# Performance work log

Hardware: AMD Instinct MI355X
Metric: run time of the kernel (lower is better)

Reference implementation:

```python
import jax, jax.numpy as jnp
import numpy as np

B, N, P, D, NH, DFFN = 4, 1024, 128, 512, 8, 2048
DH = D // NH  # 64


def setup_inputs() -> dict:
    key = jax.random.key(0)
    ks = jax.random.split(key, 64)
    i = [0]
    def rn(shape, s=1.0):
        k = ks[i[0]]; i[0] += 1
        return jax.random.normal(k, shape, jnp.float32) * s
    w = 0.05  # weight init scale
    inp = {
        "H": rn((B, N, D)),
        "V": rn((B, N, 3, D)),
        "D_batch": rn((B, N, N)),
        "rbf_bias": rn((B, 1, N, N)),  # rbf_feat_batch[layer_idx]
        "prompt_feature": rn((B * P, D)),
        # self-attn params
        "Wq": rn((4 * D, D), w), "bq": jnp.zeros((4 * D,), jnp.float32),
        "Wk": rn((4 * D, D), w), "bk": jnp.zeros((4 * D,), jnp.float32),
        "Wv": rn((D, D), w), "bv": jnp.zeros((D,), jnp.float32),
        "Wvv": rn((D, D), w),
        "Wo": rn((D, D), w), "bo": jnp.zeros((D,), jnp.float32),
        "Wvo": rn((D, D), w),
        "ln1_g": jnp.ones((D,), jnp.float32), "ln1_b": jnp.zeros((D,), jnp.float32),
        # cross-attn params (nn.MultiheadAttention packed in_proj + out_proj, then scaler_o)
        "ca_in_w": rn((3 * D, D), w), "ca_in_b": jnp.zeros((3 * D,), jnp.float32),
        "ca_out_w": rn((D, D), w), "ca_out_b": jnp.zeros((D,), jnp.float32),
        "ca_so_w": rn((D, D), w), "ca_so_b": jnp.zeros((D,), jnp.float32),
        "ln2_g": jnp.ones((D,), jnp.float32), "ln2_b": jnp.zeros((D,), jnp.float32),
        # GVP-FFN params
        "ffn_lv": rn((2 * D, D), w),
        "ffn_w1": rn((DFFN, 2 * D), w), "ffn_b1": jnp.zeros((DFFN,), jnp.float32),
        "ffn_w2": rn((2 * D, DFFN), w), "ffn_b2": jnp.zeros((2 * D,), jnp.float32),
        "ln3_g": jnp.ones((D,), jnp.float32), "ln3_b": jnp.zeros((D,), jnp.float32),
        # key-validity mask [B,N]
        "H_mask": jax.random.randint(ks[60], (B, N), 0, 2).astype(jnp.int32),
    }
    return inp


def _ln(x, g, b):
    m = x.mean(-1, keepdims=True)
    v = ((x - m) ** 2).mean(-1, keepdims=True)
    return (x - m) / jnp.sqrt(v + 1e-5) * g + b


def _ept_layer(H, V, D_batch, rbf_bias, prompt_feature,
               Wq, bq, Wk, bk, Wv, bv, Wvv, Wo, bo, Wvo, ln1_g, ln1_b,
               ca_in_w, ca_in_b, ca_out_w, ca_out_b, ca_so_w, ca_so_b, ln2_g, ln2_b,
               ffn_lv, ffn_w1, ffn_b1, ffn_w2, ffn_b2, ln3_g, ln3_b, H_mask):
    factor = 0.5 / np.sqrt(DH)
    # ---- self-attn sublayer (pre-LN on H, residual on H and V) ----
    H0, V0 = H, V
    Hn = _ln(H, ln1_g, ln1_b)
    Hq = (Hn @ Wq.T + bq).reshape(B, N, NH, 4 * DH)
    Hk = (Hn @ Wk.T + bk).reshape(B, N, NH, 4 * DH)
    Hv = (Hn @ Wv.T + bv).reshape(B, N, NH, DH)
    # vector values: [B,N,3,D] -> [B,N,3,NH,DH] -> [B,N,NH,3,DH] -> [B,N,NH,3*DH]
    Vv = (V @ Wvv.T).reshape(B, N, 3, NH, DH).transpose(0, 1, 3, 2, 4).reshape(B, N, NH, 3 * DH)
    V_attn = jnp.concatenate([Hv, Vv], axis=-1)  # [B,N,NH,4*DH]
    bias = rbf_bias + D_batch[:, None]           # [B,1,N,N]
    bias = jnp.where(H_mask[:, None, None, :] == 0, -jnp.inf, bias)
    scores = jnp.einsum('bnhd,bmhd->bhnm', Hq, Hk) * factor + bias
    attn = jax.nn.softmax(scores, axis=-1)
    res = jnp.einsum('bhnm,bmhd->bnhd', attn, V_attn)  # [B,N,NH,4*DH]
    H_res = res[..., :DH].reshape(B, N, D)
    V_res = res[..., DH:].reshape(B, N, NH, 3, DH).transpose(0, 1, 3, 2, 4).reshape(B, N, 3, D)
    H = (H_res @ Wo.T + bo) + H0
    V = (V_res @ Wvo.T) + V0
    # ---- cross-attn sublayer (pre-LN, residual on H only) ----
    H0 = H
    Hn = _ln(H, ln2_g, ln2_b)
    prompt = prompt_feature.reshape(B, P, D)
    Wq_c, Wk_c, Wv_c = ca_in_w[:D], ca_in_w[D:2 * D], ca_in_w[2 * D:]
    bq_c, bk_c, bv_c = ca_in_b[:D], ca_in_b[D:2 * D], ca_in_b[2 * D:]
    q = (Hn @ Wq_c.T + bq_c).reshape(B, N, NH, DH)
    k = (prompt @ Wk_c.T + bk_c).reshape(B, P, NH, DH)
    v = (prompt @ Wv_c.T + bv_c).reshape(B, P, NH, DH)
    ca = jax.nn.softmax(jnp.einsum('bnhd,bphd->bhnp', q, k) / np.sqrt(DH), axis=-1)
    co = jnp.einsum('bhnp,bphd->bnhd', ca, v).reshape(B, N, D)
    co = co @ ca_out_w.T + ca_out_b
    H = (co @ ca_so_w.T + ca_so_b) + H0
    # ---- GVP-FFN sublayer (pre-LN on H, residual on H and V) ----
    H0, V0 = H, V
    Hn = _ln(H, ln3_g, ln3_b)
    Vp = V @ ffn_lv.T                  # [B,N,3,2D]
    V1, V2 = Vp[..., :D], Vp[..., D:]
    scaler = jnp.concatenate([Hn, jnp.linalg.norm(V1, axis=-2)], axis=-1)  # [B,N,2D]
    h1 = jax.nn.silu(scaler @ ffn_w1.T + ffn_b1)
    so = h1 @ ffn_w2.T + ffn_b2        # [B,N,2D]
    H_out, V_upd = so[..., :D], so[..., D:]
    H = H_out + H0
    V = V_upd[..., None, :] * V2 + V0  # vector_act == 'none'
    return H, V


def reference(H, V, D_batch, rbf_bias, prompt_feature,
              Wq, bq, Wk, bk, Wv, bv, Wvv, Wo, bo, Wvo, ln1_g, ln1_b,
              ca_in_w, ca_in_b, ca_out_w, ca_out_b, ca_so_w, ca_so_b, ln2_g, ln2_b,
              ffn_lv, ffn_w1, ffn_b1, ffn_w2, ffn_b2, ln3_g, ln3_b, H_mask):
    return _ept_layer(H, V, D_batch, rbf_bias, prompt_feature,
                      Wq, bq, Wk, bk, Wv, bv, Wvv, Wo, bo, Wvo, ln1_g, ln1_b,
                      ca_in_w, ca_in_b, ca_out_w, ca_out_b, ca_so_w, ca_so_b, ln2_g, ln2_b,
                      ffn_lv, ffn_w1, ffn_b1, ffn_w2, ffn_b2, ln3_g, ln3_b, H_mask)
```

## Files before the change

### kernel.cpp

```cpp
#include <hip/hip_runtime.h>
#include <cstdint>
#include <cstddef>

#define B_    4
#define N_    1024
#define P_    128
#define D_    512
#define NH_   8

typedef unsigned short ushort_t;
typedef short short8 __attribute__((ext_vector_type(8)));
typedef float f32x4 __attribute__((ext_vector_type(4)));
typedef ushort_t ushort4_t __attribute__((ext_vector_type(4)));

__device__ inline ushort_t f2bf(float f) {
  union { float fp; unsigned int u; } v; v.fp = f;
  unsigned int r = v.u + 0x7fffu + ((v.u >> 16) & 1u);
  return (ushort_t)(r >> 16);
}
__device__ inline float bf2f(ushort_t u) {
  union { unsigned int i; float f; } v; v.i = ((unsigned int)u) << 16;
  return v.f;
}

__device__ __forceinline__ void gll16(const ushort_t* g, ushort_t* l) {
  __builtin_amdgcn_global_load_lds(
      (const __attribute__((address_space(1))) void*)g,
      (__attribute__((address_space(3))) void*)l, 16, 0, 0);
}

__device__ inline void cast8(const float* __restrict__ s, ushort_t* __restrict__ d,
                             unsigned i) {
  const float* sp = s + (size_t)i * 8;
  short8 o;
#pragma unroll
  for (int j = 0; j < 8; ++j) o[j] = (short)f2bf(sp[j]);
  *(short8*)(d + (size_t)i * 8) = o;
}

__global__ __launch_bounds__(256) void cast_fused(
    const float* s0, ushort_t* d0,  const float* s1, ushort_t* d1,
    const float* s2, ushort_t* d2,  const float* s3, ushort_t* d3,
    const float* s4, ushort_t* d4,  const float* s5, ushort_t* d5,
    const float* s6, ushort_t* d6,  const float* s7, ushort_t* d7,
    const float* s8, ushort_t* d8,  const float* s9, ushort_t* d9,
    const float* s10, ushort_t* d10, const float* s11, ushort_t* d11,
    const float* s12, ushort_t* d12, const float* s13, ushort_t* d13)
{
  unsigned i = blockIdx.x * 256 + threadIdx.x;
#define SEG(s, d, n8) if (i < (n8)) { cast8(s, d, i); return; } i -= (n8);
  SEG(s0, d0, 131072u)
  SEG(s1, d1, 131072u)
  SEG(s2, d2, 32768u)
  SEG(s3, d3, 32768u)
  SEG(s4, d4, 32768u)
  SEG(s5, d5, 32768u)
  SEG(s6, d6, 98304u)
  SEG(s7, d7, 32768u)
  SEG(s8, d8, 32768u)
  SEG(s9, d9, 65536u)
  SEG(s10, d10, 262144u)
  SEG(s11, d11, 262144u)
  SEG(s12, d12, 32768u)
  SEG(s13, d13, 786432u)
#undef SEG
}

__global__ __launch_bounds__(256) void biasmerge(const float* __restrict__ bq,
                                                 const float* __restrict__ bk,
                                                 float* __restrict__ o)
{
  int i = blockIdx.x * 256 + threadIdx.x;
  o[i] = (i < 2048) ? bq[i] : bk[i - 2048];
}

__global__ __launch_bounds__(256) void biascomb(const float* __restrict__ Db,
                                                const float* __restrict__ rbf,
                                                const int* __restrict__ mask,
                                                ushort_t* __restrict__ out)
{
  size_t i = (size_t)blockIdx.x * 256 + threadIdx.x;
  size_t e = i * 4;
  int b  = (int)(e >> 20);
  int m0 = (int)(e & 1023);
  float4 r = *(const float4*)(rbf + e);
  float4 d = *(const float4*)(Db + e);
  const int* mp = mask + b * 1024 + m0;
  ushort4_t o;
  o.x = f2bf(mp[0] ? r.x + d.x : -1e30f);
  o.y = f2bf(mp[1] ? r.y + d.y : -1e30f);
  o.z = f2bf(mp[2] ? r.z + d.z : -1e30f);
  o.w = f2bf(mp[3] ? r.w + d.w : -1e30f);
  *(ushort4_t*)(out + e) = o;
}

__global__ __launch_bounds__(256) void ln_kernel(
    const float* __restrict__ x, const float* __restrict__ g,
    const float* __restrict__ bb, ushort_t* __restrict__ y, int ostride)
{
  int row = blockIdx.x;
  int t = threadIdx.x;
  const float* xr = x + (size_t)row * D_;
  float a = xr[t], c = xr[t + 256];
  float s = a + c, sq = a * a + c * c;
#pragma unroll
  for (int off = 32; off >= 1; off >>= 1) {
    s  += __shfl_xor(s, off);
    sq += __shfl_xor(sq, off);
  }
  __shared__ float red[8];
  int w = t >> 6, lane = t & 63;
  if (lane == 0) { red[w] = s; red[4 + w] = sq; }
  __syncthreads();
  float st  = red[0] + red[1] + red[2] + red[3];
  float sqt = red[4] + red[5] + red[6] + red[7];
  float mean = st * (1.0f / D_);
  float var  = sqt * (1.0f / D_) - mean * mean;
  float inv  = rsqrtf(var + 1e-5f);
  y[(size_t)row * ostride + t]       = f2bf((a - mean) * inv * g[t] + bb[t]);
  y[(size_t)row * ostride + t + 256] = f2bf((c - mean) * inv * g[t + 256] + bb[t + 256]);
}

__global__ __launch_bounds__(256) void gemm_bf16(
    const ushort_t* __restrict__ A, const ushort_t* __restrict__ W,
    const float* __restrict__ bias, const float* __restrict__ res,
    float* __restrict__ Cf, ushort_t* __restrict__ Cb,
    int M, int N, int K, int flags)
{
  __shared__ __align__(16) ushort_t Al[128 * 32];
  __shared__ __align__(16) ushort_t Wl[128 * 32];
  const int t = threadIdx.x;
  const int wv = t >> 6, lane = t & 63, lr = lane & 15, lk = lane >> 4;
  const int wr = wv >> 1, wc = wv & 1;

  const int gx = gridDim.x;
  const int lid = blockIdx.y * gx + blockIdx.x;
  const int cpx = (gx * gridDim.y) >> 3;
  const int nlid = (lid & 7) * cpx + (lid >> 3);
  const size_t row0 = (size_t)(nlid / gx) * 128;
  const size_t col0 = (size_t)(nlid % gx) * 128;

  const int srow = 32 * wv + (lane >> 2);
  const int scol = (((lane & 3) ^ ((lane >> 3) & 3))) * 8;
  const ushort_t* ApG = A + (row0 + srow) * (size_t)K + scol;
  const ushort_t* WpG = W + (col0 + srow) * (size_t)K + scol;
  ushort_t* AlD = Al + (size_t)(32 * wv) * 32;
  ushort_t* WlD = Wl + (size_t)(32 * wv) * 32;
  const size_t K16 = (size_t)16 * K;

  f32x4 acc[4][4];
#pragma unroll
  for (int i = 0; i < 4; ++i)
#pragma unroll
    for (int j = 0; j < 4; ++j) acc[i][j] = f32x4{0.f, 0.f, 0.f, 0.f};

  const int sx = (lr >> 1) & 3;

  for (int k0 = 0; k0 < K; k0 += 32) {
    __syncthreads();
    gll16(ApG + k0,       AlD);
    gll16(ApG + k0 + K16, AlD + 512);
    gll16(WpG + k0,       WlD);
    gll16(WpG + k0 + K16, WlD + 512);
    __syncthreads();
    short8 af[4], bf[4];
#pragma unroll
    for (int i = 0; i < 4; ++i)
      af[i] = *(const short8*)&Al[(wr * 64 + i * 16 + lr) * 32 + ((lk ^ sx) << 3)];
#pragma unroll
    for (int j = 0; j < 4; ++j)
      bf[j] = *(const short8*)&Wl[(wc * 64 + j * 16 + lr) * 32 + ((lk ^ sx) << 3)];
#pragma unroll
    for (int i = 0; i < 4; ++i)
#pragma unroll
      for (int j = 0; j < 4; ++j)
        acc[i][j] = __builtin_amdgcn_mfma_f32_16x16x32_bf16(af[i], bf[j], acc[i][j], 0, 0, 0);
  }

  const int orow = wr * 64 + lk * 4, ocol = wc * 64 + lr;
#pragma unroll
  for (int i = 0; i < 4; ++i) {
#pragma unroll
    for (int j = 0; j < 4; ++j) {
      size_t colb = col0 + ocol + j * 16;
      float bv = (flags & 1) ? bias[colb] : 0.f;
#pragma unroll
      for (int r = 0; r < 4; ++r) {
        size_t rowg = row0 + orow + i * 16 + r;
        float v = acc[i][j][r] + bv;
        if (flags & 4) v = v / (1.f + __expf(-v));
        if (flags & 2) v += res[rowg * N + colb];
        if (flags & 8)  Cf[rowg * N + colb] = v;
        if (flags & 16) Cb[rowg * N + colb] = f2bf(v);
      }
    }
  }
}

__global__ __launch_bounds__(256) void gemm_bf16_sm(
    const ushort_t* __restrict__ A, const ushort_t* __restrict__ W,
    const float* __restrict__ bias, const float* __restrict__ res,
    float* __restrict__ Cf, ushort_t* __restrict__ Cb,
    int M, int N, int K, int flags)
{
  __shared__ __align__(16) ushort_t Al[64 * 32];
  __shared__ __align__(16) ushort_t Wl[128 * 32];
  const int t = threadIdx.x;
  const int wv = t >> 6, lane = t & 63, lr = lane & 15, lk = lane >> 4;
  const int wr = wv >> 1, wc = wv & 1;

  const int gx = gridDim.x;
  const int lid = blockIdx.y * gx + blockIdx.x;
  const int cpx = (gx * gridDim.y) >> 3;
  const int nlid = (lid & 7) * cpx + (lid >> 3);
  const size_t row0 = (size_t)(nlid / gx) * 64;
  const size_t col0 = (size_t)(nlid % gx) * 128;

  const int scol = (((lane & 3) ^ ((lane >> 3) & 3))) * 8;
  const int srowA = 16 * wv + (lane >> 2);
  const int srowW = 32 * wv + (lane >> 2);
  const ushort_t* ApG = A + (row0 + srowA) * (size_t)K + scol;
  const ushort_t* WpG = W + (col0 + srowW) * (size_t)K + scol;
  ushort_t* AlD = Al + (size_t)(16 * wv) * 32;
  ushort_t* WlD = Wl + (size_t)(32 * wv) * 32;
  const size_t K16 = (size_t)16 * K;

  f32x4 acc[2][4];
#pragma unroll
  for (int i = 0; i < 2; ++i)
#pragma unroll
    for (int j = 0; j < 4; ++j) acc[i][j] = f32x4{0.f, 0.f, 0.f, 0.f};

  const int sx = (lr >> 1) & 3;

  for (int k0 = 0; k0 < K; k0 += 32) {
    __syncthreads();
    gll16(ApG + k0,       AlD);
    gll16(WpG + k0,       WlD);
    gll16(WpG + k0 + K16, WlD + 512);
    __syncthreads();
    short8 af[2], bf[4];
#pragma unroll
    for (int i = 0; i < 2; ++i)
      af[i] = *(const short8*)&Al[(wr * 32 + i * 16 + lr) * 32 + ((lk ^ sx) << 3)];
#pragma unroll
    for (int j = 0; j < 4; ++j)
      bf[j] = *(const short8*)&Wl[(wc * 64 + j * 16 + lr) * 32 + ((lk ^ sx) << 3)];
#pragma unroll
    for (int i = 0; i < 2; ++i)
#pragma unroll
      for (int j = 0; j < 4; ++j)
        acc[i][j] = __builtin_amdgcn_mfma_f32_16x16x32_bf16(af[i], bf[j], acc[i][j], 0, 0, 0);
  }

  const int orow = wr * 32 + lk * 4, ocol = wc * 64 + lr;
#pragma unroll
  for (int i = 0; i < 2; ++i) {
#pragma unroll
    for (int j = 0; j < 4; ++j) {
      size_t colb = col0 + ocol + j * 16;
      float bv = (flags & 1) ? bias[colb] : 0.f;
#pragma unroll
      for (int r = 0; r < 4; ++r) {
        size_t rowg = row0 + orow + i * 16 + r;
        float v = acc[i][j][r] + bv;
        if (flags & 4) v = v / (1.f + __expf(-v));
        if (flags & 2) v += res[rowg * N + colb];
        if (flags & 8)  Cf[rowg * N + colb] = v;
        if (flags & 16) Cb[rowg * N + colb] = f2bf(v);
      }
    }
  }
}

__global__ __launch_bounds__(256) void vt_build(
    const ushort_t* __restrict__ HVb, const ushort_t* __restrict__ VVTb,
    ushort_t* __restrict__ VT)
{
  const int bh = blockIdx.z, b = bh >> 3, h = bh & 7;
  const int n0 = blockIdx.x * 64, dt = blockIdx.y;
  __shared__ __align__(16) ushort_t tile[64][72];
  const int t = threadIdx.x;
  {
    int r = t >> 2, c0 = (t & 3) * 16;
    const ushort_t* src = (dt == 0)
      ? HVb + ((size_t)(b * 1024 + n0 + r)) * 512 + h * 64 + c0
      : VVTb + (((size_t)(b * 1024 + n0 + r)) * 3 + (dt - 1)) * 512 + h * 64 + c0;
    *(short8*)&tile[r][c0]     = *(const short8*)src;
    *(short8*)&tile[r][c0 + 8] = *(const short8*)(src + 8);
  }
  __syncthreads();
  {
    int d = t >> 2, nc = (t & 3) * 16;
    short8 o0, o1;
#pragma unroll
    for (int i = 0; i < 8; ++i) { o0[i] = tile[nc + i][d]; o1[i] = tile[nc + 8 + i][d]; }
    ushort_t* dst = VT + ((size_t)bh * 256 + dt * 64 + d) * 1024 + n0 + nc;
    *(short8*)dst = o0;
    *(short8*)(dst + 8) = o1;
  }
}

__global__ __launch_bounds__(256) void attn_mfma(
    const ushort_t* __restrict__ QKg, const ushort_t* __restrict__ VTg,
    const ushort_t* __restrict__ biasb,
    ushort_t* __restrict__ HRESb, ushort_t* __restrict__ VRESb)
{
  const int bh = blockIdx.y, b = bh >> 3, h = bh & 7;
  const int q0 = blockIdx.x * 64;
  const int t = threadIdx.x, w = t >> 6, lane = t & 63, lr = lane & 15, lk = lane >> 4;

  __shared__ __align__(16) ushort_t Kl[32][264];
  __shared__ __align__(16) ushort_t Vl[256][40];
  __shared__ __align__(16) ushort_t Pl[4][16][40];

  short8 qf[8];
  {
    const ushort_t* qb = QKg + ((size_t)(b * 1024 + q0 + w * 16 + lr)) * 4096 + h * 256;
#pragma unroll
    for (int s = 0; s < 8; ++s) qf[s] = *(const short8*)(qb + s * 32 + lk * 8);
  }
  f32x4 o[16];
#pragma unroll
  for (int i = 0; i < 16; ++i) o[i] = f32x4{0.f, 0.f, 0.f, 0.f};
  float mrow[4] = {-1e30f, -1e30f, -1e30f, -1e30f};
  float lsum[4] = {0.f, 0.f, 0.f, 0.f};
  const int qrow = q0 + w * 16 + lk * 4;

  const int krow = w * 8 + (lane & 7);
  const int kc   = (lane >> 3) * 32;
  const ushort_t* ksrc = QKg + ((size_t)(b * 1024 + krow)) * 4096 + 2048 + h * 256 + kc;
  const ushort_t* vsrc = VTg + ((size_t)bh * 256 + t) * 1024;
  const int vrot = (t >> 3) & 3;

  for (int k0 = 0; k0 < 1024; k0 += 32) {
    __syncthreads();
    {
      const ushort_t* ks = ksrc + (size_t)k0 * 4096;
#pragma unroll
      for (int c = 0; c < 4; ++c)
        *(short8*)&Kl[krow][kc + c * 8] = *(const short8*)(ks + c * 8);
#pragma unroll
      for (int c = 0; c < 4; ++c) {
        int cc = (c + vrot) & 3;
        *(short8*)&Vl[t][cc * 8] = *(const short8*)(vsrc + k0 + cc * 8);
      }
    }
    __syncthreads();

    f32x4 s2[2];
    s2[0] = f32x4{0.f, 0.f, 0.f, 0.f};
    s2[1] = f32x4{0.f, 0.f, 0.f, 0.f};
    __builtin_amdgcn_s_setprio(1);
#pragma unroll
    for (int ks = 0; ks < 8; ++ks) {
#pragma unroll
      for (int j = 0; j < 2; ++j) {
        short8 kf = *(const short8*)&Kl[j * 16 + lr][ks * 32 + lk * 8];
        s2[j] = __builtin_amdgcn_mfma_f32_16x16x32_bf16(qf[ks], kf, s2[j], 0, 0, 0);
      }
    }
    __builtin_amdgcn_s_setprio(0);

    float sv[2][4];
    const ushort_t* bp = biasb + ((size_t)b << 20) + (size_t)qrow * 1024 + k0 + lr;
#pragma unroll
    for (int r = 0; r < 4; ++r) {
      sv[0][r] = s2[0][r] * 0.0625f + bf2f(bp[r * 1024]);
      sv[1][r] = s2[1][r] * 0.0625f + bf2f(bp[r * 1024 + 16]);
    }
    float pm[4], need = -1e30f;
#pragma unroll
    for (int r = 0; r < 4; ++r) {
      float m2 = fmaxf(sv[0][r], sv[1][r]);
      m2 = fmaxf(m2, __shfl_xor(m2, 1));
      m2 = fmaxf(m2, __shfl_xor(m2, 2));
      m2 = fmaxf(m2, __shfl_xor(m2, 4));
      m2 = fmaxf(m2, __shfl_xor(m2, 8));
      pm[r] = m2;
      need = fmaxf(need, m2 - mrow[r]);
    }
    if (!__all(need <= 8.f)) {
#pragma unroll
      for (int r = 0; r < 4; ++r) {
        float mn = fmaxf(mrow[r], pm[r]);
        float al = __expf(mrow[r] - mn);
        mrow[r] = mn;
        lsum[r] *= al;
#pragma unroll
        for (int d = 0; d < 16; ++d) o[d][r] *= al;
      }
    }
#pragma unroll
    for (int r = 0; r < 4; ++r) {
      float p0 = __expf(sv[0][r] - mrow[r]);
      float p1 = __expf(sv[1][r] - mrow[r]);
      float rs = p0 + p1;
      rs += __shfl_xor(rs, 1); rs += __shfl_xor(rs, 2);
      rs += __shfl_xor(rs, 4); rs += __shfl_xor(rs, 8);
      lsum[r] += rs;
      Pl[w][lk * 4 + r][lr]      = f2bf(p0);
      Pl[w][lk * 4 + r][16 + lr] = f2bf(p1);
    }
    short8 pf = *(const short8*)&Pl[w][lr][lk * 8];
    __builtin_amdgcn_s_setprio(1);
#pragma unroll
    for (int d = 0; d < 16; ++d) {
      short8 vf = *(const short8*)&Vl[d * 16 + lr][lk * 8];
      o[d] = __builtin_amdgcn_mfma_f32_16x16x32_bf16(pf, vf, o[d], 0, 0, 0);
    }
    __builtin_amdgcn_s_setprio(0);
  }

  float inv[4];
#pragma unroll
  for (int r = 0; r < 4; ++r) inv[r] = 1.f / lsum[r];
#pragma unroll
  for (int d = 0; d < 16; ++d) {
    int dcat = d * 16 + lr;
#pragma unroll
    for (int r = 0; r < 4; ++r) {
      float v = o[d][r] * inv[r];
      int n = qrow + r;
      if (dcat < 64)
        HRESb[((size_t)b * 1024 + n) * 512 + h * 64 + dcat] = f2bf(v);
      else {
        int c = (dcat - 64) >> 6, jj = (dcat - 64) & 63;
        VRESb[(((size_t)b * 1024 + n) * 3 + c) * 512 + h * 64 + jj] = f2bf(v);
      }
    }
  }
}

__global__ __launch_bounds__(256) void attn_cross_mfma(
    const ushort_t* __restrict__ Qb, const ushort_t* __restrict__ KVb,
    ushort_t* __restrict__ COb)
{
  const int bh = blockIdx.y, b = bh >> 3, h = bh & 7;
  const int q0 = blockIdx.x * 64;
  const int t = threadIdx.x, w = t >> 6, lane = t & 63, lr = lane & 15, lk = lane >> 4;

  __shared__ __align__(16) ushort_t Kl[128][72];
  __shared__ __align__(16) ushort_t Vt[64][136];
  __shared__ __align__(16) ushort_t Pl[4][16][136];

  {
    int p = t >> 1, c0 = (t & 1) * 32;
    const ushort_t* kp = KVb + ((size_t)b * 128 + p) * 1024 + h * 64 + c0;
#pragma unroll
    for (int i = 0; i < 4; ++i) {
      short8 kv = *(const short8*)(kp + i * 8);
      *(short8*)&Kl[p][c0 + i * 8] = kv;
      short8 vv = *(const short8*)(kp + 512 + i * 8);
#pragma unroll
      for (int jj = 0; jj < 8; ++jj) Vt[c0 + i * 8 + jj][p] = (ushort_t)vv[jj];
    }
  }
  __syncthreads();

  short8 qf[2];
  {
    const ushort_t* qp = Qb + ((size_t)b * 1024 + q0 + w * 16 + lr) * 512 + h * 64;
    qf[0] = *(const short8*)(qp + lk * 8);
    qf[1] = *(const short8*)(qp + 32 + lk * 8);
  }

  f32x4 s[8];
#pragma unroll
  for (int j = 0; j < 8; ++j) s[j] = f32x4{0.f, 0.f, 0.f, 0.f};
#pragma unroll
  for (int ks = 0; ks < 2; ++ks)
#pragma unroll
    for (int j = 0; j < 8; ++j) {
      short8 kf = *(const short8*)&Kl[j * 16 + lr][ks * 32 + lk * 8];
      s[j] = __builtin_amdgcn_mfma_f32_16x16x32_bf16(qf[ks], kf, s[j], 0, 0, 0);
    }

  float linv[4];
#pragma unroll
  for (int r = 0; r < 4; ++r) {
    float sc[8];
#pragma unroll
    for (int j = 0; j < 8; ++j) sc[j] = s[j][r] * 0.125f;
    float mx = sc[0];
#pragma unroll
    for (int j = 1; j < 8; ++j) mx = fmaxf(mx, sc[j]);
    mx = fmaxf(mx, __shfl_xor(mx, 1));
    mx = fmaxf(mx, __shfl_xor(mx, 2));
    mx = fmaxf(mx, __shfl_xor(mx, 4));
    mx = fmaxf(mx, __shfl_xor(mx, 8));
    float rs = 0.f;
#pragma unroll
    for (int j = 0; j < 8; ++j) {
      float p = __expf(sc[j] - mx);
      rs += p;
      Pl[w][lk * 4 + r][j * 16 + lr] = f2bf(p);
    }
    rs += __shfl_xor(rs, 1); rs += __shfl_xor(rs, 2);
    rs += __shfl_xor(rs, 4); rs += __shfl_xor(rs, 8);
    linv[r] = 1.f / rs;
  }
  __syncthreads();

  f32x4 o[4];
#pragma unroll
  for (int d = 0; d < 4; ++d) o[d] = f32x4{0.f, 0.f, 0.f, 0.f};
#pragma unroll
  for (int ks = 0; ks < 4; ++ks) {
    short8 pf = *(const short8*)&Pl[w][lr][ks * 32 + lk * 8];
#pragma unroll
    for (int d = 0; d < 4; ++d) {
      short8 vf = *(const short8*)&Vt[d * 16 + lr][ks * 32 + lk * 8];
      o[d] = __builtin_amdgcn_mfma_f32_16x16x32_bf16(pf, vf, o[d], 0, 0, 0);
    }
  }

#pragma unroll
  for (int d = 0; d < 4; ++d)
#pragma unroll
    for (int r = 0; r < 4; ++r) {
      int n = q0 + w * 16 + lk * 4 + r;
      COb[((size_t)b * 1024 + n) * 512 + h * 64 + d * 16 + lr] = f2bf(o[d][r] * linv[r]);
    }
}

__global__ __launch_bounds__(256) void vnorm_kernel(
    const ushort_t* __restrict__ Vp, ushort_t* __restrict__ scal)
{
  size_t i = (size_t)blockIdx.x * 256 + threadIdx.x;
  size_t bn = i >> 9; int d = (int)(i & 511);
  size_t base = bn * 3 * 1024 + d;
  float a = bf2f(Vp[base]);
  float b = bf2f(Vp[base + 1024]);
  float c = bf2f(Vp[base + 2048]);
  scal[bn * 1024 + 512 + d] = f2bf(sqrtf(a * a + b * b + c * c));
}

__global__ __launch_bounds__(256) void final_kernel(
    const float* __restrict__ so, const float* __restrict__ H2,
    const ushort_t* __restrict__ Vp, const float* __restrict__ Vnew,
    float* __restrict__ out)
{
  size_t i = (size_t)blockIdx.x * 256 + threadIdx.x;
  size_t bn = i >> 9; int d = (int)(i & 511);
  out[bn * 512 + d] = so[bn * 1024 + d] + H2[bn * 512 + d];
  float vu = so[bn * 1024 + 512 + d];
  float* outV = out + (size_t)B_ * N_ * D_;
#pragma unroll
  for (int c = 0; c < 3; ++c) {
    size_t vi = (bn * 3 + c) * 512 + d;
    outV[vi] = vu * bf2f(Vp[(bn * 3 + c) * 1024 + 512 + d]) + Vnew[vi];
  }
}

extern "C" void kernel_launch(void* const* d_in, const int* in_sizes, int n_in,
                              void* d_out, int out_size, void* d_ws, size_t ws_size,
                              hipStream_t stream)
{
  const float* H      = (const float*)d_in[0];
  const float* V      = (const float*)d_in[1];
  const float* Db     = (const float*)d_in[2];
  const float* rbf    = (const float*)d_in[3];
  const float* prompt = (const float*)d_in[4];
  const float* Wq  = (const float*)d_in[5];
  const float* bq  = (const float*)d_in[6];
  const float* Wk  = (const float*)d_in[7];
  const float* bk  = (const float*)d_in[8];
  const float* Wv  = (const float*)d_in[9];
  const float* bv  = (const float*)d_in[10];
  const float* Wvv = (const float*)d_in[11];
  const float* Wo  = (const float*)d_in[12];
  const float* bo  = (const float*)d_in[13];
  const float* Wvo = (const float*)d_in[14];
  const float* ln1g = (const float*)d_in[15];
  const float* ln1b = (const float*)d_in[16];
  const float* caw  = (const float*)d_in[17];
  const float* cab  = (const float*)d_in[18];
  const float* caow = (const float*)d_in[19];
  const float* caob = (const float*)d_in[20];
  const float* casw = (const float*)d_in[21];
  const float* casb = (const float*)d_in[22];
  const float* ln2g = (const float*)d_in[23];
  const float* ln2b = (const float*)d_in[24];
  const float* flv  = (const float*)d_in[25];
  const float* fw1  = (const float*)d_in[26];
  const float* fb1  = (const float*)d_in[27];
  const float* fw2  = (const float*)d_in[28];
  const float* fb2  = (const float*)d_in[29];
  const float* ln3g = (const float*)d_in[30];
  const float* ln3b = (const float*)d_in[31];
  const int*   mask = (const int*)d_in[32];

  char* wsb = (char*)d_ws;
  float* out = (float*)d_out;

#define HMB(x) ((size_t)(x) << 19)
  ushort_t* Wqkb  = (ushort_t*)(wsb + HMB(0));
  ushort_t* Wvb   = (ushort_t*)(wsb + HMB(8));
  ushort_t* Wvvb  = (ushort_t*)(wsb + HMB(9));
  ushort_t* Wob   = (ushort_t*)(wsb + HMB(10));
  ushort_t* Wvob  = (ushort_t*)(wsb + HMB(11));
  ushort_t* cawb  = (ushort_t*)(wsb + HMB(12));
  ushort_t* caowb = (ushort_t*)(wsb + HMB(15));
  ushort_t* caswb = (ushort_t*)(wsb + HMB(16));
  ushort_t* flvb  = (ushort_t*)(wsb + HMB(17));
  ushort_t* fw1b  = (ushort_t*)(wsb + HMB(19));
  ushort_t* fw2b  = (ushort_t*)(wsb + HMB(27));
  ushort_t* promptb = (ushort_t*)(wsb + HMB(35));
  float*    BQK   = (float*)   (wsb + HMB(36));
  ushort_t* HQKb  = (ushort_t*)(wsb + HMB(37));
  float*    VNEW  = (float*)   (wsb + HMB(37));
  float*    H2    = (float*)   (wsb + HMB(85));
  ushort_t* HNb   = (ushort_t*)(wsb + HMB(101));
  ushort_t* VT    = (ushort_t*)(wsb + HMB(101));
  ushort_t* QCb   = (ushort_t*)(wsb + HMB(101));
  ushort_t* KVCb  = (ushort_t*)(wsb + HMB(109));
  ushort_t* SCALb = (ushort_t*)(wsb + HMB(101));
  ushort_t* Vb    = (ushort_t*)(wsb + HMB(133));
  ushort_t* HRESb = (ushort_t*)(wsb + HMB(133));
  ushort_t* HN2b  = (ushort_t*)(wsb + HMB(133));
  ushort_t* VPb   = (ushort_t*)(wsb + HMB(133));
  ushort_t* VRESb = (ushort_t*)(wsb + HMB(141));
  ushort_t* COb   = (ushort_t*)(wsb + HMB(141));
  ushort_t* CO2b  = (ushort_t*)(wsb + HMB(149));
  ushort_t* HVb   = (ushort_t*)(wsb + HMB(157));
  ushort_t* VVTb  = (ushort_t*)(wsb + HMB(165));
  float*    H1    = (float*)   (wsb + HMB(165));
  ushort_t* BIASCb= (ushort_t*)(wsb + HMB(189));
  float*    SO    = (float*)   (wsb + HMB(189));
  ushort_t* VNEWb = (ushort_t*)(wsb + HMB(221));
  ushort_t* HH1b  = (ushort_t*)(wsb + HMB(245));

  cast_fused<<<7680, 256, 0, stream>>>(
      Wq, Wqkb, Wk, Wqkb + (size_t)2048 * 512, Wv, Wvb, Wvv, Wvvb, Wo, Wob,
      Wvo, Wvob, caw, cawb, caow, caowb, casw, caswb, flv, flvb,
      fw1, fw1b, fw2, fw2b, prompt, promptb, V, Vb);
  biasmerge<<<16, 256, 0, stream>>>(bq, bk, BQK);
  biascomb<<<4096, 256, 0, stream>>>(Db, rbf, mask, BIASCb);
  ln_kernel<<<4096, 256, 0, stream>>>(H, ln1g, ln1b, HNb, 512);

  gemm_bf16<<<dim3(32, 32), 256, 0, stream>>>(HNb, Wqkb, BQK, nullptr, nullptr, HQKb, 4096, 4096, 512, 1 | 16);
  gemm_bf16_sm<<<dim3(4, 64), 256, 0, stream>>>(HNb, Wvb, bv, nullptr, nullptr, HVb, 4096, 512, 512, 1 | 16);
  gemm_bf16<<<dim3(4, 96), 256, 0, stream>>>(Vb, Wvvb, nullptr, nullptr, nullptr, VVTb, 12288, 512, 512, 16);

  vt_build<<<dim3(16, 4, 32), 256, 0, stream>>>(HVb, VVTb, VT);

  attn_mfma<<<dim3(16, 32), 256, 0, stream>>>(HQKb, VT, BIASCb, HRESb, VRESb);

  gemm_bf16_sm<<<dim3(4, 64), 256, 0, stream>>>(HRESb, Wob, bo, H, H1, nullptr, 4096, 512, 512, 1 | 2 | 8);
  gemm_bf16<<<dim3(4, 96), 256, 0, stream>>>(VRESb, Wvob, nullptr, V, VNEW, VNEWb, 12288, 512, 512, 2 | 8 | 16);

  ln_kernel<<<4096, 256, 0, stream>>>(H1, ln2g, ln2b, HN2b, 512);
  gemm_bf16_sm<<<dim3(4, 64), 256, 0, stream>>>(HN2b, cawb, cab, nullptr, nullptr, QCb, 4096, 512, 512, 1 | 16);
  gemm_bf16_sm<<<dim3(8, 8), 256, 0, stream>>>(promptb, cawb + 262144, cab + 512, nullptr, nullptr, KVCb, 512, 1024, 512, 1 | 16);

  attn_cross_mfma<<<dim3(16, 32), 256, 0, stream>>>(QCb, KVCb, COb);

  gemm_bf16_sm<<<dim3(4, 64), 256, 0, stream>>>(COb, caowb, caob, nullptr, nullptr, CO2b, 4096, 512, 512, 1 | 16);
  gemm_bf16_sm<<<dim3(4, 64), 256, 0, stream>>>(CO2b, caswb, casb, H1, H2, nullptr, 4096, 512, 512, 1 | 2 | 8);

  gemm_bf16<<<dim3(8, 96), 256, 0, stream>>>(VNEWb, flvb, nullptr, nullptr, nullptr, VPb, 12288, 1024, 512, 16);
  ln_kernel<<<4096, 256, 0, stream>>>(H2, ln3g, ln3b, SCALb, 1024);
  vnorm_kernel<<<8192, 256, 0, stream>>>(VPb, SCALb);

  gemm_bf16<<<dim3(16, 32), 256, 0, stream>>>(SCALb, fw1b, fb1, nullptr, nullptr, HH1b, 4096, 2048, 1024, 1 | 4 | 16);
  gemm_bf16_sm<<<dim3(8, 64), 256, 0, stream>>>(HH1b, fw2b, fb2, nullptr, SO, nullptr, 4096, 1024, 2048, 1 | 8);

  final_kernel<<<8192, 256, 0, stream>>>(SO, H2, VPb, VNEW, out);

  (void)in_sizes; (void)n_in; (void)out_size; (void)ws_size;
}
```

Measured before the change: 491.8 us.

## Fuse V projection into QK GEMM and remap attention block ordering

Concatenates the Wv weights onto the packed Wq/Wk matrix so a single GEMM (N=4608) produces Q, K and H-V together, which removes one small GEMM launch and one pass over HN. The attention grid is flattened to 1D and remapped so consecutive blocks spread across batch-heads, which is meant to improve L2 locality and balance across XCDs. The K-tile load is also reindexed, and the workspace layout is reshuffled to make room for the wider QKV buffer. The risks are a strided V read in vt_build and possible aliasing mistakes in the new workspace offsets.

```diff
diff --git a/kernel.cpp b/kernel.cpp
--- a/kernel.cpp
+++ b/kernel.cpp
@@ -7,6 +7,7 @@
 #define P_    128
 #define D_    512
 #define NH_   8
+#define QKVW  4608
 
 typedef unsigned short ushort_t;
 typedef short short8 __attribute__((ext_vector_type(8)));
@@ -66,12 +67,13 @@
 #undef SEG
 }
 
-__global__ __launch_bounds__(256) void biasmerge(const float* __restrict__ bq,
-                                                 const float* __restrict__ bk,
-                                                 float* __restrict__ o)
+__global__ __launch_bounds__(256) void biasmerge3(
+    const float* __restrict__ bq, const float* __restrict__ bk,
+    const float* __restrict__ bv, float* __restrict__ o)
 {
   int i = blockIdx.x * 256 + threadIdx.x;
-  o[i] = (i < 2048) ? bq[i] : bk[i - 2048];
+  if (i >= 4608) return;
+  o[i] = (i < 2048) ? bq[i] : (i < 4096) ? bk[i - 2048] : bv[i - 4096];
 }
 
 __global__ __launch_bounds__(256) void biascomb(const float* __restrict__ Db,
@@ -274,7 +276,7 @@
 }
 
 __global__ __launch_bounds__(256) void vt_build(
-    const ushort_t* __restrict__ HVb, const ushort_t* __restrict__ VVTb,
+    const ushort_t* __restrict__ QKVb, const ushort_t* __restrict__ VVTb,
     ushort_t* __restrict__ VT)
 {
   const int bh = blockIdx.z, b = bh >> 3, h = bh & 7;
@@ -284,7 +286,7 @@
   {
     int r = t >> 2, c0 = (t & 3) * 16;
     const ushort_t* src = (dt == 0)
-      ? HVb + ((size_t)(b * 1024 + n0 + r)) * 512 + h * 64 + c0
+      ? QKVb + ((size_t)(b * 1024 + n0 + r)) * QKVW + 4096 + h * 64 + c0
       : VVTb + (((size_t)(b * 1024 + n0 + r)) * 3 + (dt - 1)) * 512 + h * 64 + c0;
     *(short8*)&tile[r][c0]     = *(const short8*)src;
     *(short8*)&tile[r][c0 + 8] = *(const short8*)(src + 8);
@@ -306,8 +308,10 @@
     const ushort_t* __restrict__ biasb,
     ushort_t* __restrict__ HRESb, ushort_t* __restrict__ VRESb)
 {
-  const int bh = blockIdx.y, b = bh >> 3, h = bh & 7;
-  const int q0 = blockIdx.x * 64;
+  const int blk = blockIdx.x;
+  const int bi = blk >> 3;
+  const int bh = (blk & 7) * 4 + (bi >> 4), b = bh >> 3, h = bh & 7;
+  const int q0 = (bi & 15) * 64;
   const int t = threadIdx.x, w = t >> 6, lane = t & 63, lr = lane & 15, lk = lane >> 4;
 
   __shared__ __align__(16) ushort_t Kl[32][264];
@@ -316,7 +320,7 @@
 
   short8 qf[8];
   {
-    const ushort_t* qb = QKg + ((size_t)(b * 1024 + q0 + w * 16 + lr)) * 4096 + h * 256;
+    const ushort_t* qb = QKg + ((size_t)(b * 1024 + q0 + w * 16 + lr)) * QKVW + h * 256;
 #pragma unroll
     for (int s = 0; s < 8; ++s) qf[s] = *(const short8*)(qb + s * 32 + lk * 8);
   }
@@ -327,16 +331,15 @@
   float lsum[4] = {0.f, 0.f, 0.f, 0.f};
   const int qrow = q0 + w * 16 + lk * 4;
 
-  const int krow = w * 8 + (lane & 7);
-  const int kc   = (lane >> 3) * 32;
-  const ushort_t* ksrc = QKg + ((size_t)(b * 1024 + krow)) * 4096 + 2048 + h * 256 + kc;
+  const int krow = t >> 3, kc = (t & 7) * 32;
+  const ushort_t* ksrc = QKg + ((size_t)(b * 1024 + krow)) * QKVW + 2048 + h * 256 + kc;
   const ushort_t* vsrc = VTg + ((size_t)bh * 256 + t) * 1024;
   const int vrot = (t >> 3) & 3;
 
   for (int k0 = 0; k0 < 1024; k0 += 32) {
     __syncthreads();
     {
-      const ushort_t* ks = ksrc + (size_t)k0 * 4096;
+      const ushort_t* ks = ksrc + (size_t)k0 * QKVW;
 #pragma unroll
       for (int c = 0; c < 4; ++c)
         *(short8*)&Kl[krow][kc + c * 8] = *(const short8*)(ks + c * 8);
@@ -595,8 +598,7 @@
   float* out = (float*)d_out;
 
 #define HMB(x) ((size_t)(x) << 19)
-  ushort_t* Wqkb  = (ushort_t*)(wsb + HMB(0));
-  ushort_t* Wvb   = (ushort_t*)(wsb + HMB(8));
+  ushort_t* Wqkvb = (ushort_t*)(wsb + HMB(0));
   ushort_t* Wvvb  = (ushort_t*)(wsb + HMB(9));
   ushort_t* Wob   = (ushort_t*)(wsb + HMB(10));
   ushort_t* Wvob  = (ushort_t*)(wsb + HMB(11));
@@ -607,45 +609,43 @@
   ushort_t* fw1b  = (ushort_t*)(wsb + HMB(19));
   ushort_t* fw2b  = (ushort_t*)(wsb + HMB(27));
   ushort_t* promptb = (ushort_t*)(wsb + HMB(35));
-  float*    BQK   = (float*)   (wsb + HMB(36));
-  ushort_t* HQKb  = (ushort_t*)(wsb + HMB(37));
+  float*    BQKV  = (float*)   (wsb + HMB(36));
+  ushort_t* HQKVb = (ushort_t*)(wsb + HMB(37));
   float*    VNEW  = (float*)   (wsb + HMB(37));
-  float*    H2    = (float*)   (wsb + HMB(85));
-  ushort_t* HNb   = (ushort_t*)(wsb + HMB(101));
-  ushort_t* VT    = (ushort_t*)(wsb + HMB(101));
-  ushort_t* QCb   = (ushort_t*)(wsb + HMB(101));
-  ushort_t* KVCb  = (ushort_t*)(wsb + HMB(109));
-  ushort_t* SCALb = (ushort_t*)(wsb + HMB(101));
+  ushort_t* VNEWb = (ushort_t*)(wsb + HMB(85));
+  float*    SO    = (float*)   (wsb + HMB(85));
+  ushort_t* VVTb  = (ushort_t*)(wsb + HMB(109));
+  ushort_t* HN2b  = (ushort_t*)(wsb + HMB(109));
+  ushort_t* QCb   = (ushort_t*)(wsb + HMB(117));
+  ushort_t* KVCb  = (ushort_t*)(wsb + HMB(125));
+  ushort_t* COb   = (ushort_t*)(wsb + HMB(127));
   ushort_t* Vb    = (ushort_t*)(wsb + HMB(133));
   ushort_t* HRESb = (ushort_t*)(wsb + HMB(133));
-  ushort_t* HN2b  = (ushort_t*)(wsb + HMB(133));
-  ushort_t* VPb   = (ushort_t*)(wsb + HMB(133));
+  ushort_t* CO2b  = (ushort_t*)(wsb + HMB(135));
   ushort_t* VRESb = (ushort_t*)(wsb + HMB(141));
-  ushort_t* COb   = (ushort_t*)(wsb + HMB(141));
-  ushort_t* CO2b  = (ushort_t*)(wsb + HMB(149));
-  ushort_t* HVb   = (ushort_t*)(wsb + HMB(157));
-  ushort_t* VVTb  = (ushort_t*)(wsb + HMB(165));
-  float*    H1    = (float*)   (wsb + HMB(165));
-  ushort_t* BIASCb= (ushort_t*)(wsb + HMB(189));
-  float*    SO    = (float*)   (wsb + HMB(189));
-  ushort_t* VNEWb = (ushort_t*)(wsb + HMB(221));
-  ushort_t* HH1b  = (ushort_t*)(wsb + HMB(245));
+  float*    H2    = (float*)   (wsb + HMB(143));
+  ushort_t* HNb   = (ushort_t*)(wsb + HMB(157));
+  ushort_t* VPb   = (ushort_t*)(wsb + HMB(159));
+  ushort_t* VT    = (ushort_t*)(wsb + HMB(165));
+  ushort_t* BIASCb= (ushort_t*)(wsb + HMB(197));
+  float*    H1    = (float*)   (wsb + HMB(213));
+  ushort_t* SCALb = (ushort_t*)(wsb + HMB(207));
+  ushort_t* HH1b  = (ushort_t*)(wsb + HMB(223));
 
   cast_fused<<<7680, 256, 0, stream>>>(
-      Wq, Wqkb, Wk, Wqkb + (size_t)2048 * 512, Wv, Wvb, Wvv, Wvvb, Wo, Wob,
-      Wvo, Wvob, caw, cawb, caow, caowb, casw, caswb, flv, flvb,
-      fw1, fw1b, fw2, fw2b, prompt, promptb, V, Vb);
-  biasmerge<<<16, 256, 0, stream>>>(bq, bk, BQK);
+      Wq, Wqkvb, Wk, Wqkvb + (size_t)2048 * 512, Wv, Wqkvb + (size_t)4096 * 512,
+      Wvv, Wvvb, Wo, Wob, Wvo, Wvob, caw, cawb, caow, caowb, casw, caswb,
+      flv, flvb, fw1, fw1b, fw2, fw2b, prompt, promptb, V, Vb);
+  biasmerge3<<<18, 256, 0, stream>>>(bq, bk, bv, BQKV);
   biascomb<<<4096, 256, 0, stream>>>(Db, rbf, mask, BIASCb);
   ln_kernel<<<4096, 256, 0, stream>>>(H, ln1g, ln1b, HNb, 512);
 
-  gemm_bf16<<<dim3(32, 32), 256, 0, stream>>>(HNb, Wqkb, BQK, nullptr, nullptr, HQKb, 4096, 4096, 512, 1 | 16);
-  gemm_bf16_sm<<<dim3(4, 64), 256, 0, stream>>>(HNb, Wvb, bv, nullptr, nullptr, HVb, 4096, 512, 512, 1 | 16);
+  gemm_bf16<<<dim3(36, 32), 256, 0, stream>>>(HNb, Wqkvb, BQKV, nullptr, nullptr, HQKVb, 4096, 4608, 512, 1 | 16);
   gemm_bf16<<<dim3(4, 96), 256, 0, stream>>>(Vb, Wvvb, nullptr, nullptr, nullptr, VVTb, 12288, 512, 512, 16);
 
-  vt_build<<<dim3(16, 4, 32), 256, 0, stream>>>(HVb, VVTb, VT);
-
-  attn_mfma<<<dim3(16, 32), 256, 0, stream>>>(HQKb, VT, BIASCb, HRESb, VRESb);
+  vt_build<<<dim3(16, 4, 32), 256, 0, stream>>>(HQKVb, VVTb, VT);
+
+  attn_mfma<<<512, 256, 0, stream>>>(HQKVb, VT, BIASCb, HRESb, VRESb);
 
   gemm_bf16_sm<<<dim3(4, 64), 256, 0, stream>>>(HRESb, Wob, bo, H, H1, nullptr, 4096, 512, 512, 1 | 2 | 8);
   gemm_bf16<<<dim3(4, 96), 256, 0, stream>>>(VRESb, Wvob, nullptr, V, VNEW, VNEWb, 12288, 512, 512, 2 | 8 | 16);
```

Result: faster. 463.0 us (-5.8%).
